# Performance work log

Hardware: AMD Instinct MI355X
Metric: run time of the kernel (lower is better)

Reference implementation:

```python
import jax, jax.numpy as jnp
import numpy as np

B, S, D = 2, 2048, 768
H = 12
HD = D // H


def setup_inputs() -> dict:
    key = jax.random.key(0)
    k1, k2, k3 = jax.random.split(key, 3)
    hidden_states = jax.random.normal(k1, (B, S, D), dtype=jnp.float32)
    Wqkv = jax.random.normal(k2, (D, 3 * D), dtype=jnp.float32) * (1.0 / np.sqrt(D))
    bqkv = jnp.zeros((3 * D,), dtype=jnp.float32)
    Wout = jax.random.normal(k3, (D, D), dtype=jnp.float32) * (1.0 / np.sqrt(D))
    bout = jnp.zeros((D,), dtype=jnp.float32)
    return {"hidden_states": hidden_states, "Wqkv": Wqkv, "bqkv": bqkv,
            "Wout": Wout, "bout": bout}


def reference(hidden_states, Wqkv, bqkv, Wout, bout):
    b, s, d = hidden_states.shape
    h, hd = H, HD
    scale = hd ** -0.5
    qkv = hidden_states @ Wqkv + bqkv                      # [b, s, 3d]
    q, k, v = jnp.split(qkv, 3, axis=-1)
    # [b, h, s, hd]
    q = q.reshape(b, s, h, hd).transpose(0, 2, 1, 3)
    k = k.reshape(b, s, h, hd).transpose(0, 2, 1, 3)
    v = v.reshape(b, s, h, hd).transpose(0, 2, 1, 3)
    scores = jnp.einsum('bhqd,bhkd->bhqk', q, k) * scale   # [b, h, s, s]
    causal = jnp.tril(jnp.ones((s, s), dtype=bool))
    scores = jnp.where(causal, scores, -jnp.inf)
    attn = jax.nn.softmax(scores, axis=-1)
    out = jnp.einsum('bhqk,bhkd->bhqd', attn, v)           # [b, h, s, hd]
    out = out.transpose(0, 2, 1, 3).reshape(b, s, d)
    return out @ Wout + bout
```

## Files before the change

kernel.cpp:

```cpp
#include <hip/hip_runtime.h>
#include <hip/hip_bf16.h>

typedef __attribute__((ext_vector_type(8))) short bf16x8;
typedef __attribute__((ext_vector_type(4))) float f32x4;
typedef __attribute__((ext_vector_type(4))) unsigned int u32x4;

#define NB 2
#define NS 2048
#define ND 768
#define NH 12
#define NHD 64
#define N3D 2304
#define NM (NB * NS)

__device__ __forceinline__ unsigned short f2bf(float x) {
    union { float f; unsigned u; } v; v.f = x;
    unsigned r = v.u + 0x7FFFu + ((v.u >> 16) & 1u);
    return (unsigned short)(r >> 16);
}

__device__ __forceinline__ unsigned cvt_pk_bf16(float lo, float hi) {
    unsigned r;
    asm volatile("v_cvt_pk_bf16_f32 %0, %1, %2" : "=v"(r) : "v"(lo), "v"(hi));
    return r;
}

__device__ __forceinline__ void transp_tile(const float* __restrict__ in,
                                            unsigned short* __restrict__ out,
                                            int K, int N, int nt, int kt,
                                            float (*T)[33]) {
    const int n0 = nt * 32, k0 = kt * 32;
    const int r = threadIdx.x >> 3, c4 = (threadIdx.x & 7) * 4;
    float4 v = *reinterpret_cast<const float4*>(&in[(size_t)(k0 + r) * N + n0 + c4]);
    T[r][c4 + 0] = v.x; T[r][c4 + 1] = v.y; T[r][c4 + 2] = v.z; T[r][c4 + 3] = v.w;
    __syncthreads();
    ushort4 o;
    o.x = f2bf(T[c4 + 0][r]); o.y = f2bf(T[c4 + 1][r]);
    o.z = f2bf(T[c4 + 2][r]); o.w = f2bf(T[c4 + 3][r]);
    *reinterpret_cast<ushort4*>(&out[(size_t)(n0 + r) * K + k0 + c4]) = o;
}

__global__ __launch_bounds__(256)
void prep(const float* __restrict__ hs, unsigned short* __restrict__ hsb,
          const float* __restrict__ Wqkv, unsigned short* __restrict__ W1t,
          const float* __restrict__ Wout, unsigned short* __restrict__ W2t) {
    __shared__ float T[32][33];
    const int bid = blockIdx.x;
    if (bid < 3072) {
        const int i = (bid * 256 + threadIdx.x) * 4;
        float4 v = *reinterpret_cast<const float4*>(hs + i);
        ushort4 o;
        o.x = f2bf(v.x); o.y = f2bf(v.y); o.z = f2bf(v.z); o.w = f2bf(v.w);
        *reinterpret_cast<ushort4*>(hsb + i) = o;
    } else if (bid < 3072 + 1728) {
        const int idx = bid - 3072;
        transp_tile(Wqkv, W1t, ND, N3D, idx % 72, idx / 72, T);
    } else {
        const int idx = bid - 4800;
        transp_tile(Wout, W2t, ND, ND, idx % 24, idx / 24, T);
    }
}

template<int BM, int BN, int EPI>
__global__ __launch_bounds__(256)
void gemm_k768(const unsigned short* __restrict__ A,
               const unsigned short* __restrict__ Bt,
               const float* __restrict__ bias,
               unsigned short* __restrict__ Qo, unsigned short* __restrict__ Ko,
               unsigned short* __restrict__ Vto, float* __restrict__ Co) {
    __shared__ unsigned short SMEM[(BM + BN) * 64];
    unsigned short* As = SMEM;
    unsigned short* Bs = SMEM + BM * 64;
    const int t = threadIdx.x;
    const int wv = t >> 6, lane = t & 63;
    const int lr = lane & 15, lg = lane >> 4;
    const int wr = wv >> 1, wc = wv & 1;
    const int m0 = blockIdx.y * BM;
    const int n0 = blockIdx.x * BN;
    constexpr int FM = BM / 32;
    constexpr int FN = BN / 32;

    f32x4 acc[FM][FN];
#pragma unroll
    for (int i = 0; i < FM; ++i)
#pragma unroll
        for (int j = 0; j < FN; ++j) acc[i][j] = (f32x4){0.f, 0.f, 0.f, 0.f};

    const int sr = t >> 3;
    const int sb = t & 7;

    for (int ki = 0; ki < ND / 64; ++ki) {
        const int k0 = ki * 64;
        __syncthreads();
#pragma unroll
        for (int jj = 0; jj < BM / 32; ++jj) {
            const int row = jj * 32 + sr;
            __builtin_amdgcn_global_load_lds(
                (const void*)(A + (size_t)(m0 + row) * ND + k0 + ((sb ^ (row & 7)) * 8)),
                (void*)(As + jj * 2048 + wv * 512), 16, 0, 0);
        }
#pragma unroll
        for (int jj = 0; jj < BN / 32; ++jj) {
            const int row = jj * 32 + sr;
            __builtin_amdgcn_global_load_lds(
                (const void*)(Bt + (size_t)(n0 + row) * ND + k0 + ((sb ^ (row & 7)) * 8)),
                (void*)(Bs + jj * 2048 + wv * 512), 16, 0, 0);
        }
        __syncthreads();
#pragma unroll
        for (int kc = 0; kc < 2; ++kc) {
            bf16x8 af[FM], bfr[FN];
#pragma unroll
            for (int mi = 0; mi < FM; ++mi) {
                const int row = wr * (BM / 2) + mi * 16 + lr;
                af[mi] = *(const bf16x8*)&As[row * 64 + (((kc * 4 + lg) ^ (row & 7)) * 8)];
            }
#pragma unroll
            for (int nj = 0; nj < FN; ++nj) {
                const int row = wc * (BN / 2) + nj * 16 + lr;
                bfr[nj] = *(const bf16x8*)&Bs[row * 64 + (((kc * 4 + lg) ^ (row & 7)) * 8)];
            }
#pragma unroll
            for (int mi = 0; mi < FM; ++mi)
#pragma unroll
                for (int nj = 0; nj < FN; ++nj)
                    acc[mi][nj] = __builtin_amdgcn_mfma_f32_16x16x32_bf16(
                        af[mi], bfr[nj], acc[mi][nj], 0, 0, 0);
        }
    }

    if (EPI == 0) {
        const int sec = n0 / ND;
        if (sec < 2) {
#pragma unroll
            for (int mi = 0; mi < FM; ++mi) {
#pragma unroll
                for (int nj = 0; nj < FN; ++nj) {
                    const int n = n0 + wc * (BN / 2) + nj * 16 + lr;
                    const int rem = n - sec * ND;
                    const int hh = rem >> 6, dd = rem & 63;
                    const float b = bias[n];
#pragma unroll
                    for (int r = 0; r < 4; ++r) {
                        const int m = m0 + wr * (BM / 2) + mi * 16 + lg * 4 + r;
                        const int bb = m >> 11, ss = m & (NS - 1);
                        const int bhh = bb * NH + hh;
                        const float v = acc[mi][nj][r] + b;
                        if (sec == 0)
                            Qo[((size_t)bhh * NS + ss) * NHD + dd] = f2bf(v * 0.18033688011112042f);
                        else
                            Ko[((size_t)bhh * NS + ss) * NHD + dd] = f2bf(v);
                    }
                }
            }
        } else {
            __syncthreads();
            char* Tb = reinterpret_cast<char*>(SMEM);
#pragma unroll
            for (int mi = 0; mi < FM; ++mi) {
#pragma unroll
                for (int nj = 0; nj < FN; ++nj) {
                    const int n_l = wc * (BN / 2) + nj * 16 + lr;
                    const int m_l = wr * (BM / 2) + mi * 16 + lg * 4;
                    const float b = bias[n0 + n_l];
                    ushort4 pk;
                    pk.x = f2bf(acc[mi][nj][0] + b);
                    pk.y = f2bf(acc[mi][nj][1] + b);
                    pk.z = f2bf(acc[mi][nj][2] + b);
                    pk.w = f2bf(acc[mi][nj][3] + b);
                    const int off = n_l * 256 + (((m_l * 2) ^ ((n_l & 15) << 4)));
                    *reinterpret_cast<ushort4*>(Tb + off) = pk;
                }
            }
            __syncthreads();
            const int bb = m0 >> 11;
            const int ssb = m0 & (NS - 1);
#pragma unroll
            for (int h = 0; h < (BN * 16) / 256; ++h) {
                const int p = t + 256 * h;
                const int n_l = p >> 4, j = p & 15;
                const int off = n_l * 256 + (((j ^ (n_l & 15)) << 4));
                bf16x8 v = *reinterpret_cast<const bf16x8*>(Tb + off);
                const int rem = n0 + n_l - 2 * ND;
                const int hh = rem >> 6, dd = rem & 63;
                const int bhh = bb * NH + hh;
                *reinterpret_cast<bf16x8*>(Vto + ((size_t)(bhh * NHD + dd)) * NS + ssb + 8 * j) = v;
            }
        }
    } else {
#pragma unroll
        for (int mi = 0; mi < FM; ++mi)
#pragma unroll
            for (int nj = 0; nj < FN; ++nj) {
                const int n = n0 + wc * (BN / 2) + nj * 16 + lr;
                const float b = bias[n];
#pragma unroll
                for (int r = 0; r < 4; ++r) {
                    const int m = m0 + wr * (BM / 2) + mi * 16 + lg * 4 + r;
                    Co[(size_t)m * ND + n] = acc[mi][nj][r] + b;
                }
            }
    }
}

__global__ __launch_bounds__(256)
void attn_mfma(const unsigned short* __restrict__ Qg,
               const unsigned short* __restrict__ Kg,
               const unsigned short* __restrict__ Vtg,
               unsigned short* __restrict__ AO) {
    __shared__ unsigned short Ks[2][64 * 64];
    __shared__ unsigned short Vs[2][64 * 64];
    const int n = blockIdx.x;
    const int x = n & 7, ii = n >> 3;
    const int bh = ((ii >> 5) << 3) + x;
    const int qt = (31 - (ii & 31) + 11 * (ii >> 5)) & 31;
    const int t = threadIdx.x;
    const int w = t >> 6, lane = t & 63;
    const int lr = lane & 15, lg = lane >> 4;
    const int lgp = lg & 1;
    const int qrow = qt * 64 + w * 16 + lr;
    const size_t bhoff = (size_t)bh * (NS * NHD);

    const unsigned short* Qp = Qg + bhoff + (size_t)qrow * NHD;
    const bf16x8 qB0 = *(const bf16x8*)(Qp + lg * 8);
    const bf16x8 qB1 = *(const bf16x8*)(Qp + 32 + lg * 8);

    float m_run = -1e30f, l_part = 0.f;
    f32x4 of[4];
#pragma unroll
    for (int f = 0; f < 4; ++f) of[f] = (f32x4){0.f, 0.f, 0.f, 0.f};

    const unsigned short* Kb = Kg + bhoff;
    const unsigned short* Vb = Vtg + bhoff;
    const int srow = lane >> 3, sblk = lane & 7;
    const int ntiles = qt + 1;
    const int bswz = ((lg & 1) << 1) | (lg >> 1);

#define STAGE(buf, kv0)                                                           \
    {                                                                             \
        _Pragma("unroll")                                                         \
        for (int h = 0; h < 2; ++h) {                                             \
            const int rr = w * 16 + h * 8 + srow;                                 \
            __builtin_amdgcn_global_load_lds(                                     \
                (const void*)(Kb + (size_t)((kv0) + rr) * NHD + ((sblk ^ (rr & 7)) * 8)),  \
                (void*)(Ks[buf] + (w * 16 + h * 8) * 64), 16, 0, 0);              \
            __builtin_amdgcn_global_load_lds(                                     \
                (const void*)(Vb + (size_t)rr * NS + (kv0) + ((sblk ^ (rr & 7)) * 8)),     \
                (void*)(Vs[buf] + (w * 16 + h * 8) * 64), 16, 0, 0);              \
        }                                                                         \
    }

    STAGE(0, 0);
    for (int kt = 0; kt < ntiles; ++kt) {
        __syncthreads();
        if (kt + 1 < ntiles) STAGE((kt + 1) & 1, (kt + 1) * 64);
        const unsigned short* Kc = Ks[kt & 1];
        const unsigned short* Vc = Vs[kt & 1];
        const int kv0 = kt * 64;

        f32x4 sf[4];
#pragma unroll
        for (int f = 0; f < 4; ++f) sf[f] = (f32x4){0.f, 0.f, 0.f, 0.f};
        __builtin_amdgcn_s_setprio(1);
#pragma unroll
        for (int f = 0; f < 4; ++f) {
            const int krow = f * 16 + lr;
            const bf16x8 a0 = *(const bf16x8*)&Kc[krow * 64 + ((lg ^ (krow & 7)) * 8)];
            const bf16x8 a1 = *(const bf16x8*)&Kc[krow * 64 + (((4 + lg) ^ (krow & 7)) * 8)];
            sf[f] = __builtin_amdgcn_mfma_f32_16x16x32_bf16(a0, qB0, sf[f], 0, 0, 0);
            sf[f] = __builtin_amdgcn_mfma_f32_16x16x32_bf16(a1, qB1, sf[f], 0, 0, 0);
        }
        __builtin_amdgcn_s_setprio(0);

        if (kt == ntiles - 1) {
            const int thr = qrow - kv0;
#pragma unroll
            for (int f = 0; f < 4; ++f)
#pragma unroll
                for (int r = 0; r < 4; ++r)
                    if (f * 16 + lg * 4 + r > thr) sf[f][r] = -1e30f;
        }

        float tm = -1e30f;
#pragma unroll
        for (int f = 0; f < 4; ++f)
            tm = fmaxf(tm, fmaxf(fmaxf(sf[f][0], sf[f][1]), fmaxf(sf[f][2], sf[f][3])));
        tm = fmaxf(tm, __shfl_xor(tm, 16));
        tm = fmaxf(tm, __shfl_xor(tm, 32));
        if (!__all(tm <= m_run)) {
            const float nm = fmaxf(m_run, tm);
            const float corr = exp2f(m_run - nm);
            m_run = nm;
            l_part *= corr;
#pragma unroll
            for (int f = 0; f < 4; ++f)
#pragma unroll
                for (int r = 0; r < 4; ++r) of[f][r] *= corr;
        }
#pragma unroll
        for (int f = 0; f < 4; ++f)
#pragma unroll
            for (int r = 0; r < 4; ++r) {
                sf[f][r] = exp2f(sf[f][r] - m_run);
                l_part += sf[f][r];
            }

        bf16x8 pb[2];
#pragma unroll
        for (int c = 0; c < 2; ++c) {
            const unsigned A0 = cvt_pk_bf16(sf[2 * c][0], sf[2 * c][1]);
            const unsigned A1 = cvt_pk_bf16(sf[2 * c][2], sf[2 * c][3]);
            const unsigned B0 = cvt_pk_bf16(sf[2 * c + 1][0], sf[2 * c + 1][1]);
            const unsigned B1 = cvt_pk_bf16(sf[2 * c + 1][2], sf[2 * c + 1][3]);
            const unsigned s0 = lgp ? A0 : B0;
            const unsigned s1 = lgp ? A1 : B1;
            const unsigned r0 = (unsigned)__shfl_xor((int)s0, 16);
            const unsigned r1 = (unsigned)__shfl_xor((int)s1, 16);
            const unsigned o0 = lgp ? B0 : A0;
            const unsigned o1 = lgp ? B1 : A1;
            u32x4 wvv;
            wvv[0] = lgp ? r0 : o0;
            wvv[1] = lgp ? r1 : o1;
            wvv[2] = lgp ? o0 : r0;
            wvv[3] = lgp ? o1 : r1;
            pb[c] = __builtin_bit_cast(bf16x8, wvv);
        }

        __builtin_amdgcn_s_setprio(1);
#pragma unroll
        for (int fA = 0; fA < 4; ++fA) {
            const int drow = fA * 16 + lr;
#pragma unroll
            for (int c = 0; c < 2; ++c) {
                const int blk = 4 * c + bswz;
                const bf16x8 va = *(const bf16x8*)&Vc[drow * 64 + ((blk ^ (drow & 7)) * 8)];
                of[fA] = __builtin_amdgcn_mfma_f32_16x16x32_bf16(va, pb[c], of[fA], 0, 0, 0);
            }
        }
        __builtin_amdgcn_s_setprio(0);
    }
#undef STAGE

    l_part += __shfl_xor(l_part, 16);
    l_part += __shfl_xor(l_part, 32);
    const float inv = 1.f / l_part;
    const int bb = bh / NH, hh = bh - bb * NH;
    unsigned short* op = AO + ((size_t)(bb * NS + qrow)) * ND + hh * NHD;
#pragma unroll
    for (int fA = 0; fA < 4; ++fA) {
        ushort4 o4;
        o4.x = f2bf(of[fA][0] * inv);
        o4.y = f2bf(of[fA][1] * inv);
        o4.z = f2bf(of[fA][2] * inv);
        o4.w = f2bf(of[fA][3] * inv);
        *reinterpret_cast<ushort4*>(op + fA * 16 + lg * 4) = o4;
    }
}

extern "C" void kernel_launch(void* const* d_in, const int* in_sizes, int n_in,
                              void* d_out, int out_size, void* d_ws, size_t ws_size,
                              hipStream_t stream) {
    const float* hs   = (const float*)d_in[0];
    const float* Wqkv = (const float*)d_in[1];
    const float* bqkv = (const float*)d_in[2];
    const float* Wout = (const float*)d_in[3];
    const float* bout = (const float*)d_in[4];
    float* out = (float*)d_out;

    char* wp = (char*)d_ws;
    unsigned short* hsb = (unsigned short*)wp; wp += (size_t)NM * ND * 2;
    unsigned short* W1t = (unsigned short*)wp; wp += (size_t)N3D * ND * 2;
    unsigned short* W2t = (unsigned short*)wp; wp += (size_t)ND * ND * 2;
    const size_t per = (size_t)NB * NH * NS * NHD;
    unsigned short* Qb  = (unsigned short*)wp; wp += per * 2;
    unsigned short* Kb  = (unsigned short*)wp; wp += per * 2;
    unsigned short* Vtb = (unsigned short*)wp; wp += per * 2;
    unsigned short* AOb = (unsigned short*)wp; wp += per * 2;

    prep<<<3072 + 1728 + 576, 256, 0, stream>>>(hs, hsb, Wqkv, W1t, Wout, W2t);

    gemm_k768<128, 96, 0><<<dim3(N3D / 96, NM / 128), 256, 0, stream>>>(
        hsb, W1t, bqkv, Qb, Kb, Vtb, nullptr);

    attn_mfma<<<dim3(NS / 64 * NB * NH), 256, 0, stream>>>(Qb, Kb, Vtb, AOb);

    gemm_k768<64, 64, 1><<<dim3(ND / 64, NM / 64), 256, 0, stream>>>(
        AOb, W2t, bout, nullptr, nullptr, nullptr, out);
}
```

Measured before the change: 165.7 us.

## Restructure causal attention into paired 32-row query tiles with split-KV waves

The attention kernel now handles two 32-row query tiles per block, pairing a long and a short causal tile (63-jp and jp) so every block does about the same work. Each pair of waves splits each 128-key chunk into two 64-key halves, and the two partial softmax states are merged through shared memory at the end. K is double-buffered in 128-row chunks, V is single-buffered, and the exp calls use raw v_exp_f32. This aims to fix causal load imbalance and raise per-block parallelism, at the cost of extra __syncthreads, a merge step, and idle waves on diagonal chunks.

```diff
diff --git a/kernel.cpp b/kernel.cpp
--- a/kernel.cpp
+++ b/kernel.cpp
@@ -22,6 +22,12 @@
 __device__ __forceinline__ unsigned cvt_pk_bf16(float lo, float hi) {
     unsigned r;
     asm volatile("v_cvt_pk_bf16_f32 %0, %1, %2" : "=v"(r) : "v"(lo), "v"(hi));
+    return r;
+}
+
+__device__ __forceinline__ float fexp2(float x) {
+    float r;
+    asm("v_exp_f32 %0, %1" : "=v"(r) : "v"(x));
     return r;
 }
 
@@ -177,8 +183,8 @@
             const int ssb = m0 & (NS - 1);
 #pragma unroll
             for (int h = 0; h < (BN * 16) / 256; ++h) {
-                const int p = t + 256 * h;
-                const int n_l = p >> 4, j = p & 15;
+                const int pp = t + 256 * h;
+                const int n_l = pp >> 4, j = pp & 15;
                 const int off = n_l * 256 + (((j ^ (n_l & 15)) << 4));
                 bf16x8 v = *reinterpret_cast<const bf16x8*>(Tb + off);
                 const int rem = n0 + n_l - 2 * ND;
@@ -208,153 +214,194 @@
                const unsigned short* __restrict__ Kg,
                const unsigned short* __restrict__ Vtg,
                unsigned short* __restrict__ AO) {
-    __shared__ unsigned short Ks[2][64 * 64];
-    __shared__ unsigned short Vs[2][64 * 64];
+    __shared__ unsigned short Ks[2][128 * 64];
+    __shared__ unsigned short Vs[64 * 128];
+    float* MRG = reinterpret_cast<float*>(Vs);
+
     const int n = blockIdx.x;
     const int x = n & 7, ii = n >> 3;
     const int bh = ((ii >> 5) << 3) + x;
-    const int qt = (31 - (ii & 31) + 11 * (ii >> 5)) & 31;
+    const int jp = ii & 31;
     const int t = threadIdx.x;
     const int w = t >> 6, lane = t & 63;
     const int lr = lane & 15, lg = lane >> 4;
     const int lgp = lg & 1;
-    const int qrow = qt * 64 + w * 16 + lr;
+    const int qh = w & 1, p = w >> 1;
     const size_t bhoff = (size_t)bh * (NS * NHD);
-
-    const unsigned short* Qp = Qg + bhoff + (size_t)qrow * NHD;
-    const bf16x8 qB0 = *(const bf16x8*)(Qp + lg * 8);
-    const bf16x8 qB1 = *(const bf16x8*)(Qp + 32 + lg * 8);
-
-    float m_run = -1e30f, l_part = 0.f;
-    f32x4 of[4];
-#pragma unroll
-    for (int f = 0; f < 4; ++f) of[f] = (f32x4){0.f, 0.f, 0.f, 0.f};
-
     const unsigned short* Kb = Kg + bhoff;
     const unsigned short* Vb = Vtg + bhoff;
-    const int srow = lane >> 3, sblk = lane & 7;
-    const int ntiles = qt + 1;
     const int bswz = ((lg & 1) << 1) | (lg >> 1);
-
-#define STAGE(buf, kv0)                                                           \
-    {                                                                             \
-        _Pragma("unroll")                                                         \
-        for (int h = 0; h < 2; ++h) {                                             \
-            const int rr = w * 16 + h * 8 + srow;                                 \
-            __builtin_amdgcn_global_load_lds(                                     \
-                (const void*)(Kb + (size_t)((kv0) + rr) * NHD + ((sblk ^ (rr & 7)) * 8)),  \
-                (void*)(Ks[buf] + (w * 16 + h * 8) * 64), 16, 0, 0);              \
-            __builtin_amdgcn_global_load_lds(                                     \
-                (const void*)(Vb + (size_t)rr * NS + (kv0) + ((sblk ^ (rr & 7)) * 8)),     \
-                (void*)(Vs[buf] + (w * 16 + h * 8) * 64), 16, 0, 0);              \
-        }                                                                         \
-    }
-
-    STAGE(0, 0);
-    for (int kt = 0; kt < ntiles; ++kt) {
+    const int ksr = lane >> 3, ksb = lane & 7;
+    const int vsr = lane >> 4, vsb = lane & 15;
+    const int bb = bh / NH, hh = bh - bb * NH;
+
+#define STAGEK(buf, kvb)                                                        \
+    {                                                                           \
+        _Pragma("unroll")                                                       \
+        for (int g = 0; g < 4; ++g) {                                           \
+            const int row = g * 32 + w * 8 + ksr;                               \
+            __builtin_amdgcn_global_load_lds(                                   \
+                (const void*)(Kb + (size_t)((kvb) + row) * NHD + ((ksb ^ (row & 7)) * 8)), \
+                (void*)(Ks[buf] + (g * 32 + w * 8) * 64), 16, 0, 0);            \
+        }                                                                       \
+    }
+#define STAGEV(kvb)                                                             \
+    {                                                                           \
+        _Pragma("unroll")                                                       \
+        for (int g = 0; g < 4; ++g) {                                           \
+            const int d = g * 16 + w * 4 + vsr;                                 \
+            __builtin_amdgcn_global_load_lds(                                   \
+                (const void*)(Vb + (size_t)d * NS + (kvb) + ((vsb ^ (d & 7)) * 8)), \
+                (void*)(Vs + (g * 16 + w * 4) * 128), 16, 0, 0);                \
+        }                                                                       \
+    }
+
+#pragma unroll 1
+    for (int mem = 0; mem < 2; ++mem) {
+        const int qtile = mem ? jp : 63 - jp;
+        const int q0 = qtile * 32;
+        const int nr = qtile / 4 + 1;
+        const int qrow = q0 + qh * 16 + lr;
+
+        const unsigned short* Qp = Qg + bhoff + (size_t)qrow * NHD;
+        const bf16x8 qB0 = *(const bf16x8*)(Qp + lg * 8);
+        const bf16x8 qB1 = *(const bf16x8*)(Qp + 32 + lg * 8);
+
+        float m_run = -1e30f, l_part = 0.f;
+        f32x4 of[4];
+#pragma unroll
+        for (int f = 0; f < 4; ++f) of[f] = (f32x4){0.f, 0.f, 0.f, 0.f};
+
+        STAGEK(0, 0);
         __syncthreads();
-        if (kt + 1 < ntiles) STAGE((kt + 1) & 1, (kt + 1) * 64);
-        const unsigned short* Kc = Ks[kt & 1];
-        const unsigned short* Vc = Vs[kt & 1];
-        const int kv0 = kt * 64;
-
-        f32x4 sf[4];
-#pragma unroll
-        for (int f = 0; f < 4; ++f) sf[f] = (f32x4){0.f, 0.f, 0.f, 0.f};
-        __builtin_amdgcn_s_setprio(1);
-#pragma unroll
-        for (int f = 0; f < 4; ++f) {
-            const int krow = f * 16 + lr;
-            const bf16x8 a0 = *(const bf16x8*)&Kc[krow * 64 + ((lg ^ (krow & 7)) * 8)];
-            const bf16x8 a1 = *(const bf16x8*)&Kc[krow * 64 + (((4 + lg) ^ (krow & 7)) * 8)];
-            sf[f] = __builtin_amdgcn_mfma_f32_16x16x32_bf16(a0, qB0, sf[f], 0, 0, 0);
-            sf[f] = __builtin_amdgcn_mfma_f32_16x16x32_bf16(a1, qB1, sf[f], 0, 0, 0);
-        }
-        __builtin_amdgcn_s_setprio(0);
-
-        if (kt == ntiles - 1) {
-            const int thr = qrow - kv0;
+#pragma unroll 1
+        for (int R = 0; R < nr; ++R) {
+            STAGEV(R * 128);
+            if (R + 1 < nr) STAGEK((R + 1) & 1, (R + 1) * 128);
+            const unsigned short* Kc = Ks[R & 1];
+            const int kvw = R * 128 + p * 64;
+            const bool active = kvw <= q0 + 31;
+
+            f32x4 sf[4];
+            bf16x8 pb[2];
+            if (active) {
+#pragma unroll
+                for (int f = 0; f < 4; ++f) sf[f] = (f32x4){0.f, 0.f, 0.f, 0.f};
+                __builtin_amdgcn_s_setprio(1);
+#pragma unroll
+                for (int f = 0; f < 4; ++f) {
+                    const int krow = p * 64 + f * 16 + lr;
+                    const bf16x8 a0 = *(const bf16x8*)&Kc[krow * 64 + ((lg ^ (krow & 7)) * 8)];
+                    const bf16x8 a1 = *(const bf16x8*)&Kc[krow * 64 + (((4 + lg) ^ (krow & 7)) * 8)];
+                    sf[f] = __builtin_amdgcn_mfma_f32_16x16x32_bf16(a0, qB0, sf[f], 0, 0, 0);
+                    sf[f] = __builtin_amdgcn_mfma_f32_16x16x32_bf16(a1, qB1, sf[f], 0, 0, 0);
+                }
+                __builtin_amdgcn_s_setprio(0);
+
+                const int rel = qrow - kvw;
+                if (rel < 63) {
+#pragma unroll
+                    for (int f = 0; f < 4; ++f)
+#pragma unroll
+                        for (int r = 0; r < 4; ++r)
+                            if (f * 16 + lg * 4 + r > rel) sf[f][r] = -1e30f;
+                }
+
+                float tm = -1e30f;
+#pragma unroll
+                for (int f = 0; f < 4; ++f)
+                    tm = fmaxf(tm, fmaxf(fmaxf(sf[f][0], sf[f][1]), fmaxf(sf[f][2], sf[f][3])));
+                tm = fmaxf(tm, __shfl_xor(tm, 16));
+                tm = fmaxf(tm, __shfl_xor(tm, 32));
+                if (!__all(tm <= m_run)) {
+                    const float nm = fmaxf(m_run, tm);
+                    const float corr = fexp2(m_run - nm);
+                    m_run = nm;
+                    l_part *= corr;
+#pragma unroll
+                    for (int f = 0; f < 4; ++f)
+#pragma unroll
+                        for (int r = 0; r < 4; ++r) of[f][r] *= corr;
+                }
+#pragma unroll
+                for (int f = 0; f < 4; ++f)
+#pragma unroll
+                    for (int r = 0; r < 4; ++r) {
+                        sf[f][r] = fexp2(sf[f][r] - m_run);
+                        l_part += sf[f][r];
+                    }
+
+#pragma unroll
+                for (int c = 0; c < 2; ++c) {
+                    const unsigned A0 = cvt_pk_bf16(sf[2 * c][0], sf[2 * c][1]);
+                    const unsigned A1 = cvt_pk_bf16(sf[2 * c][2], sf[2 * c][3]);
+                    const unsigned B0 = cvt_pk_bf16(sf[2 * c + 1][0], sf[2 * c + 1][1]);
+                    const unsigned B1 = cvt_pk_bf16(sf[2 * c + 1][2], sf[2 * c + 1][3]);
+                    const unsigned s0 = lgp ? A0 : B0;
+                    const unsigned s1 = lgp ? A1 : B1;
+                    const unsigned r0 = (unsigned)__shfl_xor((int)s0, 16);
+                    const unsigned r1 = (unsigned)__shfl_xor((int)s1, 16);
+                    const unsigned o0 = lgp ? B0 : A0;
+                    const unsigned o1 = lgp ? B1 : A1;
+                    u32x4 wvv;
+                    wvv[0] = lgp ? r0 : o0;
+                    wvv[1] = lgp ? r1 : o1;
+                    wvv[2] = lgp ? o0 : r0;
+                    wvv[3] = lgp ? o1 : r1;
+                    pb[c] = __builtin_bit_cast(bf16x8, wvv);
+                }
+            }
+            __syncthreads();
+            if (active) {
+                __builtin_amdgcn_s_setprio(1);
+#pragma unroll
+                for (int fA = 0; fA < 4; ++fA) {
+                    const int drow = fA * 16 + lr;
+#pragma unroll
+                    for (int c = 0; c < 2; ++c) {
+                        const int blk = p * 8 + 4 * c + bswz;
+                        const bf16x8 va = *(const bf16x8*)&Vs[drow * 128 + ((blk ^ (drow & 7)) * 8)];
+                        of[fA] = __builtin_amdgcn_mfma_f32_16x16x32_bf16(va, pb[c], of[fA], 0, 0, 0);
+                    }
+                }
+                __builtin_amdgcn_s_setprio(0);
+            }
+            __syncthreads();
+        }
+
+        l_part += __shfl_xor(l_part, 16);
+        l_part += __shfl_xor(l_part, 32);
+        if (p == 1) {
+            float* mr = &MRG[(qh * 64 + lane) * 18];
+            mr[0] = m_run; mr[1] = l_part;
 #pragma unroll
             for (int f = 0; f < 4; ++f)
 #pragma unroll
-                for (int r = 0; r < 4; ++r)
-                    if (f * 16 + lg * 4 + r > thr) sf[f][r] = -1e30f;
-        }
-
-        float tm = -1e30f;
-#pragma unroll
-        for (int f = 0; f < 4; ++f)
-            tm = fmaxf(tm, fmaxf(fmaxf(sf[f][0], sf[f][1]), fmaxf(sf[f][2], sf[f][3])));
-        tm = fmaxf(tm, __shfl_xor(tm, 16));
-        tm = fmaxf(tm, __shfl_xor(tm, 32));
-        if (!__all(tm <= m_run)) {
-            const float nm = fmaxf(m_run, tm);
-            const float corr = exp2f(m_run - nm);
-            m_run = nm;
-            l_part *= corr;
-#pragma unroll
-            for (int f = 0; f < 4; ++f)
-#pragma unroll
-                for (int r = 0; r < 4; ++r) of[f][r] *= corr;
-        }
-#pragma unroll
-        for (int f = 0; f < 4; ++f)
-#pragma unroll
-            for (int r = 0; r < 4; ++r) {
-                sf[f][r] = exp2f(sf[f][r] - m_run);
-                l_part += sf[f][r];
-            }
-
-        bf16x8 pb[2];
-#pragma unroll
-        for (int c = 0; c < 2; ++c) {
-            const unsigned A0 = cvt_pk_bf16(sf[2 * c][0], sf[2 * c][1]);
-            const unsigned A1 = cvt_pk_bf16(sf[2 * c][2], sf[2 * c][3]);
-            const unsigned B0 = cvt_pk_bf16(sf[2 * c + 1][0], sf[2 * c + 1][1]);
-            const unsigned B1 = cvt_pk_bf16(sf[2 * c + 1][2], sf[2 * c + 1][3]);
-            const unsigned s0 = lgp ? A0 : B0;
-            const unsigned s1 = lgp ? A1 : B1;
-            const unsigned r0 = (unsigned)__shfl_xor((int)s0, 16);
-            const unsigned r1 = (unsigned)__shfl_xor((int)s1, 16);
-            const unsigned o0 = lgp ? B0 : A0;
-            const unsigned o1 = lgp ? B1 : A1;
-            u32x4 wvv;
-            wvv[0] = lgp ? r0 : o0;
-            wvv[1] = lgp ? r1 : o1;
-            wvv[2] = lgp ? o0 : r0;
-            wvv[3] = lgp ? o1 : r1;
-            pb[c] = __builtin_bit_cast(bf16x8, wvv);
-        }
-
-        __builtin_amdgcn_s_setprio(1);
-#pragma unroll
-        for (int fA = 0; fA < 4; ++fA) {
-            const int drow = fA * 16 + lr;
-#pragma unroll
-            for (int c = 0; c < 2; ++c) {
-                const int blk = 4 * c + bswz;
-                const bf16x8 va = *(const bf16x8*)&Vc[drow * 64 + ((blk ^ (drow & 7)) * 8)];
-                of[fA] = __builtin_amdgcn_mfma_f32_16x16x32_bf16(va, pb[c], of[fA], 0, 0, 0);
-            }
-        }
-        __builtin_amdgcn_s_setprio(0);
-    }
-#undef STAGE
-
-    l_part += __shfl_xor(l_part, 16);
-    l_part += __shfl_xor(l_part, 32);
-    const float inv = 1.f / l_part;
-    const int bb = bh / NH, hh = bh - bb * NH;
-    unsigned short* op = AO + ((size_t)(bb * NS + qrow)) * ND + hh * NHD;
-#pragma unroll
-    for (int fA = 0; fA < 4; ++fA) {
-        ushort4 o4;
-        o4.x = f2bf(of[fA][0] * inv);
-        o4.y = f2bf(of[fA][1] * inv);
-        o4.z = f2bf(of[fA][2] * inv);
-        o4.w = f2bf(of[fA][3] * inv);
-        *reinterpret_cast<ushort4*>(op + fA * 16 + lg * 4) = o4;
-    }
+                for (int r = 0; r < 4; ++r) mr[2 + f * 4 + r] = of[f][r];
+        }
+        __syncthreads();
+        if (p == 0) {
+            const float* mr = &MRG[(qh * 64 + lane) * 18];
+            const float m1 = mr[0], l1 = mr[1];
+            const float mm = fmaxf(m_run, m1);
+            const float a0 = fexp2(m_run - mm);
+            const float a1 = fexp2(m1 - mm);
+            const float inv = 1.f / (l_part * a0 + l1 * a1);
+            unsigned short* op = AO + ((size_t)(bb * NS + qrow)) * ND + hh * NHD;
+#pragma unroll
+            for (int fA = 0; fA < 4; ++fA) {
+                ushort4 o4;
+                o4.x = f2bf((of[fA][0] * a0 + mr[2 + fA * 4 + 0] * a1) * inv);
+                o4.y = f2bf((of[fA][1] * a0 + mr[2 + fA * 4 + 1] * a1) * inv);
+                o4.z = f2bf((of[fA][2] * a0 + mr[2 + fA * 4 + 2] * a1) * inv);
+                o4.w = f2bf((of[fA][3] * a0 + mr[2 + fA * 4 + 3] * a1) * inv);
+                *reinterpret_cast<ushort4*>(op + fA * 16 + lg * 4) = o4;
+            }
+        }
+        __syncthreads();
+    }
+#undef STAGEK
+#undef STAGEV
 }
 
 extern "C" void kernel_launch(void* const* d_in, const int* in_sizes, int n_in,
@@ -382,7 +429,7 @@
     gemm_k768<128, 96, 0><<<dim3(N3D / 96, NM / 128), 256, 0, stream>>>(
         hsb, W1t, bqkv, Qb, Kb, Vtb, nullptr);
 
-    attn_mfma<<<dim3(NS / 64 * NB * NH), 256, 0, stream>>>(Qb, Kb, Vtb, AOb);
+    attn_mfma<<<768, 256, 0, stream>>>(Qb, Kb, Vtb, AOb);
 
     gemm_k768<64, 64, 1><<<dim3(ND / 64, NM / 64), 256, 0, stream>>>(
         AOb, W2t, bout, nullptr, nullptr, nullptr, out);
```

Result: faster. 155.3 us (-6.3%).
